# Kernel tuning notes

Hardware: AMD Instinct MI355X
Metric: run time of the kernel (lower is better)

Reference implementation:

```python
import jax, jax.numpy as jnp
import numpy as np

B, L, D_IN, D_H, N_CLS = 512, 256, 300, 96, 20
N = B * L            # total nodes = 131072
DEG = 8
E = N * DEG          # 1,048,576 edges
VOCAB = 50001        # num_words + 1 (padding row)
STEP = 2
NEG_SLOPE = 0.2


def setup_inputs() -> dict:
    key = jax.random.key(0)
    ks = jax.random.split(key, 24)
    node_ids = jax.random.randint(ks[0], (N,), 0, 50000)
    # block-local edges: each edge stays within its graph's node range
    gid = jnp.repeat(jnp.arange(B), L * DEG)           # [E]
    src = gid * L + jax.random.randint(ks[1], (E,), 0, L)
    dst = gid * L + jax.random.randint(ks[2], (E,), 0, L)

    def xavier(k, shape):
        fan_in, fan_out = shape[0], shape[-1]
        a = float(np.sqrt(6.0 / (fan_in + fan_out)))
        return jax.random.uniform(k, shape, jnp.float32, -a, a)

    inp = {
        "node_ids": node_ids, "src": src, "dst": dst,
        "embed": jax.random.normal(ks[3], (VOCAB, D_IN), jnp.float32),
        "We": xavier(ks[4], (D_IN, D_H)), "be": jnp.zeros((D_H,), jnp.float32),
        "Wg": xavier(ks[5], (D_H, D_H)),
        "att_src": xavier(ks[6], (D_H,)), "att_dst": xavier(ks[7], (D_H,)),
        "bg": jnp.zeros((D_H,), jnp.float32),
        "Wz0": xavier(ks[8], (D_H, D_H)), "bz0": jnp.zeros((D_H,), jnp.float32),
        "Wz1": xavier(ks[9], (D_H, D_H)), "bz1": jnp.zeros((D_H,), jnp.float32),
        "Wr0": xavier(ks[10], (D_H, D_H)), "br0": jnp.zeros((D_H,), jnp.float32),
        "Wr1": xavier(ks[11], (D_H, D_H)), "br1": jnp.zeros((D_H,), jnp.float32),
        "Wh0": xavier(ks[12], (D_H, D_H)), "bh0": jnp.zeros((D_H,), jnp.float32),
        "Wh1": xavier(ks[13], (D_H, D_H)), "bh1": jnp.zeros((D_H,), jnp.float32),
        "Wemb": xavier(ks[14], (D_H, D_H)),
        "Wmlp": xavier(ks[15], (D_H, N_CLS)),
    }
    return inp


def _forward(node_ids, src, dst, embed, We, be, Wg, att_src, att_dst, bg,
             Wz0, bz0, Wz1, bz1, Wr0, br0, Wr1, br1, Wh0, bh0, Wh1, bh1,
             Wemb, Wmlp):
    # embedding lookup + encode (dropout off, eval)
    x = embed[node_ids]                                  # [N, D_IN]
    x = jnp.tanh(x @ We + be)                            # [N, D_H]

    # self loops (GATConv add_self_loops=True, heads=1)
    loop = jnp.arange(N)
    s = jnp.concatenate([src, loop])
    d = jnp.concatenate([dst, loop])

    for _ in range(STEP):
        # ---- GATConv ----
        h = x @ Wg                                       # [N, D_H]
        a_s = h @ att_src                                # [N]
        a_d = h @ att_dst                                # [N]
        e = a_s[s] + a_d[d]
        e = jnp.where(e > 0, e, NEG_SLOPE * e)           # leaky_relu
        # segment softmax over incoming edges of each target node
        m = jax.ops.segment_max(e, d, num_segments=N)
        ex = jnp.exp(e - m[d])
        denom = jax.ops.segment_sum(ex, d, num_segments=N)
        alpha = ex / denom[d]                            # [E+N]
        a = jax.ops.segment_sum(alpha[:, None] * h[s], d, num_segments=N) + bg
        # ---- GRU update (act=tanh) ----
        z = jax.nn.sigmoid(a @ Wz0 + bz0 + x @ Wz1 + bz1)
        r = jax.nn.sigmoid(a @ Wr0 + br0 + x @ Wr1 + br1)
        hh = jnp.tanh(a @ Wh0 + bh0 + (x * r) @ Wh1 + bh1)
        x = hh * z + x * (1.0 - z)

    # graph2batch: equal-length graphs -> reshape, mask is all ones
    xb = x.reshape(B, L, D_H)
    y = jnp.tanh(xb @ Wemb)                              # [B, L, D_H]
    pooled = y.max(axis=1) + y.mean(axis=1)              # max + mean readout
    return pooled @ Wmlp                                 # [B, N_CLS]


def reference(node_ids, src, dst, embed, We, be, Wg, att_src, att_dst, bg,
              Wz0, bz0, Wz1, bz1, Wr0, br0, Wr1, br1, Wh0, bh0, Wh1, bh1,
              Wemb, Wmlp):
    return _forward(node_ids, src, dst, embed, We, be, Wg, att_src, att_dst, bg,
                    Wz0, bz0, Wz1, bz1, Wr0, br0, Wr1, br1, Wh0, bh0, Wh1, bh1,
                    Wemb, Wmlp)
```

## Files before the change

kernel.cpp:

```cpp
#include <hip/hip_runtime.h>
#include <hip/hip_bf16.h>

#define NNODES 131072
#define LGRAPH 256
#define BGRAPH 512
#define DIN 300
#define DH 96
#define EPG 2048
#define VOCAB 50001
#define NCLS 20
#define NEG 0.2f
#define EMB_ROWS 50048
#define EMB_K 320
#define WS 100
#define XS 104

typedef __attribute__((ext_vector_type(4))) float f32x4;
typedef __attribute__((ext_vector_type(8))) short bf16x8;
typedef __attribute__((ext_vector_type(8))) unsigned short u16x8;
#define MFMA16(a, b, c) __builtin_amdgcn_mfma_f32_16x16x32_bf16(a, b, c, 0, 0, 0)

__device__ __forceinline__ unsigned short f2b(float f) {
  __hip_bfloat16 h = __float2bfloat16(f);
  return *reinterpret_cast<unsigned short*>(&h);
}
__device__ __forceinline__ float b2f(unsigned short u) {
  unsigned v = ((unsigned)u) << 16;
  return __uint_as_float(v);
}
__device__ __forceinline__ float sigm(float v) { return 1.f / (1.f + __expf(-v)); }
__device__ __forceinline__ float ftanh(float x) {
  float ax = fabsf(x);
  float e = __expf(ax + ax);
  float t = 1.f - 2.f / (e + 1.f);
  return copysignf(t, x);
}

__global__ void k_prep_w(const float* __restrict__ Wg, const float* __restrict__ Wz0,
                         const float* __restrict__ Wz1, const float* __restrict__ Wr0,
                         const float* __restrict__ Wr1, const float* __restrict__ Wh0,
                         const float* __restrict__ Wh1, const float* __restrict__ Wemb,
                         const float* __restrict__ We,
                         const float* __restrict__ bz0, const float* __restrict__ bz1,
                         const float* __restrict__ br0, const float* __restrict__ br1,
                         const float* __restrict__ bh0, const float* __restrict__ bh1,
                         unsigned short* __restrict__ WT, unsigned short* __restrict__ WeT,
                         float* __restrict__ bc) {
  const int b = blockIdx.x, t = threadIdx.x;
  if (b < 8) {
    const float* src = (b == 0) ? Wg : (b == 1) ? Wz0 : (b == 2) ? Wz1 : (b == 3) ? Wr0
                     : (b == 4) ? Wr1 : (b == 5) ? Wh0 : (b == 6) ? Wh1 : Wemb;
    unsigned short* dst = WT + b * DH * DH;
    for (int i = t; i < DH * DH; i += 256) {
      int c = i / DH, k = i - c * DH;
      dst[i] = f2b(src[k * DH + c]);
    }
  } else if (b == 8) {
    for (int i = t; i < DH * EMB_K; i += 256) {
      int c = i / EMB_K, k = i - c * EMB_K;
      WeT[i] = (k < DIN) ? f2b(We[k * DH + c]) : (unsigned short)0;
    }
  } else {
    if (t < DH) {
      bc[t] = bz0[t] + bz1[t];
      bc[DH + t] = br0[t] + br1[t];
      bc[2 * DH + t] = bh0[t] + bh1[t];
    }
  }
}

__device__ __forceinline__ bf16x8 ldcvt(const float* __restrict__ p, int row, int ko) {
  bf16x8 r;
  if (row < VOCAB) {
    float4 c0 = (ko + 4 <= DIN) ? *(const float4*)&p[row * DIN + ko]
                                : make_float4(0.f, 0.f, 0.f, 0.f);
    float4 c1 = (ko + 8 <= DIN) ? *(const float4*)&p[row * DIN + ko + 4]
                                : make_float4(0.f, 0.f, 0.f, 0.f);
    r[0] = (short)f2b(c0.x); r[1] = (short)f2b(c0.y);
    r[2] = (short)f2b(c0.z); r[3] = (short)f2b(c0.w);
    r[4] = (short)f2b(c1.x); r[5] = (short)f2b(c1.y);
    r[6] = (short)f2b(c1.z); r[7] = (short)f2b(c1.w);
  } else {
    #pragma unroll
    for (int j = 0; j < 8; ++j) r[j] = 0;
  }
  return r;
}

__global__ void k_emb_mm(const float* __restrict__ embed,
                         const unsigned short* __restrict__ WeT,
                         unsigned short* __restrict__ Tb) {
  const int t = threadIdx.x, w = t >> 6, l = t & 63, li = l & 15, lh = l >> 4;
  const int wbase = blockIdx.x * 128 + w * 32;
  f32x4 acc[2][6];
  #pragma unroll
  for (int rt = 0; rt < 2; rt++)
    #pragma unroll
    for (int ct = 0; ct < 6; ct++) acc[rt][ct] = (f32x4)0.f;
  for (int ks = 0; ks < 10; ++ks) {
    const int ko = lh * 8 + ks * 32;
    bf16x8 aA0 = ldcvt(embed, wbase + li, ko);
    bf16x8 aA1 = ldcvt(embed, wbase + 16 + li, ko);
    #pragma unroll
    for (int ct = 0; ct < 6; ct++) {
      bf16x8 bB = *(const bf16x8*)&WeT[(ct * 16 + li) * EMB_K + ko];
      acc[0][ct] = MFMA16(aA0, bB, acc[0][ct]);
      acc[1][ct] = MFMA16(aA1, bB, acc[1][ct]);
    }
  }
  #pragma unroll
  for (int rt = 0; rt < 2; rt++)
    #pragma unroll
    for (int ct = 0; ct < 6; ct++)
      #pragma unroll
      for (int r = 0; r < 4; r++)
        Tb[(wbase + rt * 16 + lh * 4 + r) * DH + ct * 16 + li] = f2b(acc[rt][ct][r]);
}

__global__ __launch_bounds__(256) void k_gh(
    const int* __restrict__ ids, const unsigned short* __restrict__ Tb,
    const float* __restrict__ be, const unsigned short* __restrict__ WgT,
    const float* __restrict__ att_s, const float* __restrict__ att_d,
    unsigned short* __restrict__ xb, unsigned short* __restrict__ h,
    float* __restrict__ a_s, float* __restrict__ a_d) {
  __shared__ __align__(16) unsigned short sX[128 * XS];
  __shared__ int s_id[128];
  __shared__ float s_be[DH];
  const int t = threadIdx.x, w = t >> 6, l = t & 63, li = l & 15, lh = l >> 4;
  const int nb0 = blockIdx.x * 128;
  bf16x8 WF[6][3];
  #pragma unroll
  for (int ct = 0; ct < 6; ++ct)
    #pragma unroll
    for (int ks = 0; ks < 3; ++ks)
      WF[ct][ks] = *(const bf16x8*)&WgT[(ct * 16 + li) * DH + lh * 8 + ks * 32];
  if (t < 128) s_id[t] = ids[nb0 + t];
  if (t < DH) s_be[t] = be[t];
  __syncthreads();
  #pragma unroll
  for (int j = 0; j < 6; ++j) {
    int idx = t + 256 * j;
    int row = idx / 12, ch = idx - row * 12;
    u16x8 v = *(const u16x8*)&Tb[s_id[row] * DH + ch * 8];
    u16x8 o;
    #pragma unroll
    for (int k = 0; k < 8; ++k) o[k] = f2b(ftanh(b2f(v[k]) + s_be[ch * 8 + k]));
    *(u16x8*)&sX[row * XS + ch * 8] = o;
    *(u16x8*)&xb[(nb0 + row) * DH + ch * 8] = o;
  }
  __syncthreads();
  const int wbase = w * 32;
  f32x4 acc[2][6];
  #pragma unroll
  for (int rt = 0; rt < 2; rt++)
    #pragma unroll
    for (int ct = 0; ct < 6; ct++) acc[rt][ct] = (f32x4)0.f;
  bf16x8 aA[2][3];
  #pragma unroll
  for (int rt = 0; rt < 2; rt++)
    #pragma unroll
    for (int ks = 0; ks < 3; ks++)
      aA[rt][ks] = *(const bf16x8*)&sX[(wbase + rt * 16 + li) * XS + lh * 8 + ks * 32];
  #pragma unroll
  for (int ks = 0; ks < 3; ++ks)
    #pragma unroll
    for (int ct = 0; ct < 6; ct++) {
      acc[0][ct] = MFMA16(aA[0][ks], WF[ct][ks], acc[0][ct]);
      acc[1][ct] = MFMA16(aA[1][ks], WF[ct][ks], acc[1][ct]);
    }
  float ps[2][4] = {}, pd[2][4] = {};
  #pragma unroll
  for (int rt = 0; rt < 2; rt++)
    #pragma unroll
    for (int ct = 0; ct < 6; ct++) {
      const int col = ct * 16 + li;
      const float as_ = att_s[col], ad_ = att_d[col];
      #pragma unroll
      for (int r = 0; r < 4; r++) {
        float v = acc[rt][ct][r];
        h[(nb0 + wbase + rt * 16 + lh * 4 + r) * DH + col] = f2b(v);
        ps[rt][r] += v * as_;
        pd[rt][r] += v * ad_;
      }
    }
  #pragma unroll
  for (int rt = 0; rt < 2; rt++)
    #pragma unroll
    for (int r = 0; r < 4; r++) {
      float s = ps[rt][r], d = pd[rt][r];
      #pragma unroll
      for (int m = 1; m < 16; m <<= 1) { s += __shfl_xor(s, m); d += __shfl_xor(d, m); }
      if (li == 0) {
        const int row = nb0 + wbase + rt * 16 + lh * 4 + r;
        a_s[row] = s;
        a_d[row] = d;
      }
    }
}

__global__ __launch_bounds__(256) void k_h(
    const unsigned short* __restrict__ xb, const unsigned short* __restrict__ WgT,
    const float* __restrict__ att_s, const float* __restrict__ att_d,
    unsigned short* __restrict__ h, float* __restrict__ a_s,
    float* __restrict__ a_d) {
  __shared__ __align__(16) unsigned short sW[DH * WS];
  const int t = threadIdx.x, w = t >> 6, l = t & 63, li = l & 15, lh = l >> 4;
  const int wbase = blockIdx.x * 128 + w * 32;
  for (int i = t; i < DH * 12; i += 256) {
    int r = i / 12, c8 = i - r * 12;
    *(int4*)&sW[r * WS + c8 * 8] = *(const int4*)&WgT[r * DH + c8 * 8];
  }
  __syncthreads();
  f32x4 acc[2][6];
  #pragma unroll
  for (int rt = 0; rt < 2; rt++)
    #pragma unroll
    for (int ct = 0; ct < 6; ct++) acc[rt][ct] = (f32x4)0.f;
  #pragma unroll
  for (int ks = 0; ks < 3; ++ks) {
    const int ko = lh * 8 + ks * 32;
    bf16x8 aA0 = *(const bf16x8*)&xb[(wbase + li) * DH + ko];
    bf16x8 aA1 = *(const bf16x8*)&xb[(wbase + 16 + li) * DH + ko];
    #pragma unroll
    for (int ct = 0; ct < 6; ct++) {
      bf16x8 bB = *(const bf16x8*)&sW[(ct * 16 + li) * WS + ko];
      acc[0][ct] = MFMA16(aA0, bB, acc[0][ct]);
      acc[1][ct] = MFMA16(aA1, bB, acc[1][ct]);
    }
  }
  float ps[2][4] = {}, pd[2][4] = {};
  #pragma unroll
  for (int rt = 0; rt < 2; rt++)
    #pragma unroll
    for (int ct = 0; ct < 6; ct++) {
      const int col = ct * 16 + li;
      const float as_ = att_s[col], ad_ = att_d[col];
      #pragma unroll
      for (int r = 0; r < 4; r++) {
        float v = acc[rt][ct][r];
        h[(wbase + rt * 16 + lh * 4 + r) * DH + col] = f2b(v);
        ps[rt][r] += v * as_;
        pd[rt][r] += v * ad_;
      }
    }
  #pragma unroll
  for (int rt = 0; rt < 2; rt++)
    #pragma unroll
    for (int r = 0; r < 4; r++) {
      float s = ps[rt][r], d = pd[rt][r];
      #pragma unroll
      for (int m = 1; m < 16; m <<= 1) { s += __shfl_xor(s, m); d += __shfl_xor(d, m); }
      if (li == 0) {
        const int row = wbase + rt * 16 + lh * 4 + r;
        a_s[row] = s;
        a_d[row] = d;
      }
    }
}

__global__ __launch_bounds__(512, 4) void k_att(
    const int* __restrict__ src, const int* __restrict__ dst,
    const unsigned short* __restrict__ h, const float* __restrict__ a_sg,
    const float* __restrict__ a_dg, const float* __restrict__ bg,
    unsigned short* __restrict__ aout) {
  __shared__ __align__(16) unsigned short sH[LGRAPH * XS];
  __shared__ float s_ev[EPG];
  __shared__ unsigned char s_sl[EPG], s_dl[EPG];
  __shared__ unsigned char s_srcS[EPG];
  __shared__ int s_cnt[LGRAPH], s_off[LGRAPH], s_pos[LGRAPH];
  __shared__ float s_as[LGRAPH], s_ad[LGRAPH];
  __shared__ float s_bg[DH];
  const int g = blockIdx.x, t = threadIdx.x;
  const int nb = g * LGRAPH;
  if (t < LGRAPH) { s_cnt[t] = 0; s_as[t] = a_sg[nb + t]; s_ad[t] = a_dg[nb + t]; }
  if (t < DH) s_bg[t] = bg[t];
  #pragma unroll
  for (int j = 0; j < 6; ++j) {
    int idx = t + 512 * j;
    int row = idx / 12, ch = idx - row * 12;
    *(int4*)&sH[row * XS + ch * 8] = *(const int4*)&h[(nb + row) * DH + ch * 8];
  }
  __syncthreads();
  for (int e = t; e < EPG; e += 512) {
    int sl = src[g * EPG + e] - nb, dl = dst[g * EPG + e] - nb;
    s_sl[e] = (unsigned char)sl;
    s_dl[e] = (unsigned char)dl;
    atomicAdd(&s_cnt[dl], 1);
  }
  __syncthreads();
  if (t < 64) {
    int carry = 0;
    #pragma unroll
    for (int c = 0; c < 4; ++c) {
      int v = s_cnt[c * 64 + t];
      int x = v;
      #pragma unroll
      for (int o = 1; o < 64; o <<= 1) {
        int y = __shfl_up(x, o);
        if (t >= o) x += y;
      }
      s_off[c * 64 + t] = x - v + carry;
      carry += __shfl(x, 63);
    }
  }
  __syncthreads();
  if (t < LGRAPH) s_pos[t] = s_off[t];
  __syncthreads();
  for (int e = t; e < EPG; e += 512) {
    int sl = s_sl[e], dl = s_dl[e];
    float ee = s_as[sl] + s_ad[dl];
    ee = ee > 0.f ? ee : NEG * ee;
    int pos = atomicAdd(&s_pos[dl], 1);
    s_srcS[pos] = (unsigned char)sl;
    s_ev[pos] = ee;
  }
  __syncthreads();
  {
    const int d = t >> 1, half = t & 1;
    const int beg = s_off[d], end = beg + s_cnt[d];
    float ss = s_as[d] + s_ad[d];
    ss = ss > 0.f ? ss : NEG * ss;
    float m = ss;
    for (int i = beg; i < end; ++i) m = fmaxf(m, s_ev[i]);
    const int cbase = half * 48;
    float acc[48];
    float wself = __expf(ss - m);
    float den = wself;
    #pragma unroll
    for (int k = 0; k < 6; ++k) {
      u16x8 v = *(const u16x8*)&sH[d * XS + cbase + k * 8];
      #pragma unroll
      for (int j = 0; j < 8; ++j) acc[k * 8 + j] = wself * b2f(v[j]);
    }
    for (int i = beg; i < end; ++i) {
      float wv = __expf(s_ev[i] - m);
      den += wv;
      int sl2 = s_srcS[i];
      #pragma unroll
      for (int k = 0; k < 6; ++k) {
        u16x8 v = *(const u16x8*)&sH[sl2 * XS + cbase + k * 8];
        #pragma unroll
        for (int j = 0; j < 8; ++j) acc[k * 8 + j] += wv * b2f(v[j]);
      }
    }
    float inv = 1.f / den;
    unsigned short* op = &aout[(nb + d) * DH + cbase];
    #pragma unroll
    for (int k = 0; k < 6; ++k) {
      u16x8 o;
      #pragma unroll
      for (int j = 0; j < 8; ++j) o[j] = f2b(acc[k * 8 + j] * inv + s_bg[cbase + k * 8 + j]);
      *(u16x8*)&op[k * 8] = o;
    }
  }
}

__global__ __launch_bounds__(768, 3) void k_gru(
    const unsigned short* __restrict__ ab, unsigned short* __restrict__ xb,
    const unsigned short* __restrict__ WT, const float* __restrict__ bc) {
  __shared__ __align__(16) unsigned short sW[6 * DH * WS];
  __shared__ __align__(16) unsigned short sX[128 * WS];
  const int t = threadIdx.x, w = t >> 6, l = t & 63, li = l & 15, lh = l >> 4;
  const int wr = w / 3, wc = w - wr * 3;
  #pragma unroll
  for (int m = 0; m < 6; ++m) {
    const int srcm = (m == 0) ? 3 : (m == 1) ? 4 : (m == 2) ? 1 : (m == 3) ? 2 : (m == 4) ? 5 : 6;
    const unsigned short* srcp = WT + srcm * DH * DH;
    for (int i = t; i < DH * 12; i += 768) {
      int r = i / 12, c8 = i - r * 12;
      *(int4*)&sW[(m * DH + r) * WS + c8 * 8] = *(const int4*)&srcp[r * DH + c8 * 8];
    }
  }
  float zb_[2], rb_[2], hb_[2];
  #pragma unroll
  for (int ct = 0; ct < 2; ++ct) {
    const int col = wc * 32 + ct * 16 + li;
    zb_[ct] = bc[col]; rb_[ct] = bc[DH + col]; hb_[ct] = bc[2 * DH + col];
  }

  for (int tile = 0; tile < 4; ++tile) {
    const int nb0 = (blockIdx.x * 4 + tile) * 128;
    __syncthreads();
    #pragma unroll
    for (int j = 0; j < 2; ++j) {
      int idx = t + 768 * j;
      int row = idx / 12, ch = idx - row * 12;
      *(int4*)&sX[row * WS + ch * 8] = *(const int4*)&xb[(nb0 + row) * DH + ch * 8];
    }
    __syncthreads();
    bf16x8 aA[2][3], aX[2][3];
    #pragma unroll
    for (int rt = 0; rt < 2; rt++)
      #pragma unroll
      for (int ks = 0; ks < 3; ks++) {
        const int row = wr * 32 + rt * 16 + li;
        const int ko = lh * 8 + ks * 32;
        aA[rt][ks] = *(const bf16x8*)&ab[(nb0 + row) * DH + ko];
        aX[rt][ks] = *(const bf16x8*)&sX[row * WS + ko];
      }
    float xo[2][2][4];
    #pragma unroll
    for (int rt = 0; rt < 2; rt++)
      #pragma unroll
      for (int ct = 0; ct < 2; ct++)
        #pragma unroll
        for (int r = 0; r < 4; r++)
          xo[rt][ct][r] = b2f(sX[(wr * 32 + rt * 16 + lh * 4 + r) * WS + wc * 32 + ct * 16 + li]);
    f32x4 accR[2][2], accZ[2][2];
    #pragma unroll
    for (int rt = 0; rt < 2; rt++)
      #pragma unroll
      for (int ct = 0; ct < 2; ct++) { accR[rt][ct] = (f32x4)0.f; accZ[rt][ct] = (f32x4)0.f; }
    #pragma unroll
    for (int ks = 0; ks < 3; ks++) {
      const int ko = lh * 8 + ks * 32;
      #pragma unroll
      for (int ct = 0; ct < 2; ct++) {
        const int wrow = wc * 32 + ct * 16 + li;
        bf16x8 w_r0 = *(const bf16x8*)&sW[(0 * DH + wrow) * WS + ko];
        bf16x8 w_r1 = *(const bf16x8*)&sW[(1 * DH + wrow) * WS + ko];
        bf16x8 w_z0 = *(const bf16x8*)&sW[(2 * DH + wrow) * WS + ko];
        bf16x8 w_z1 = *(const bf16x8*)&sW[(3 * DH + wrow) * WS + ko];
        #pragma unroll
        for (int rt = 0; rt < 2; rt++) {
          accR[rt][ct] = MFMA16(aA[rt][ks], w_r0, accR[rt][ct]);
          accR[rt][ct] = MFMA16(aX[rt][ks], w_r1, accR[rt][ct]);
          accZ[rt][ct] = MFMA16(aA[rt][ks], w_z0, accZ[rt][ct]);
          accZ[rt][ct] = MFMA16(aX[rt][ks], w_z1, accZ[rt][ct]);
        }
      }
    }
    __syncthreads();
    #pragma unroll
    for (int rt = 0; rt < 2; rt++)
      #pragma unroll
      for (int ct = 0; ct < 2; ct++) {
        const int col = wc * 32 + ct * 16 + li;
        #pragma unroll
        for (int r = 0; r < 4; r++) {
          float rv = sigm(accR[rt][ct][r] + rb_[ct]);
          sX[(wr * 32 + rt * 16 + lh * 4 + r) * WS + col] = f2b(xo[rt][ct][r] * rv);
        }
      }
    __syncthreads();
    bf16x8 aU[2][3];
    #pragma unroll
    for (int rt = 0; rt < 2; rt++)
      #pragma unroll
      for (int ks = 0; ks < 3; ks++)
        aU[rt][ks] = *(const bf16x8*)&sX[(wr * 32 + rt * 16 + li) * WS + lh * 8 + ks * 32];
    __syncthreads();
    f32x4 accH[2][2];
    #pragma unroll
    for (int rt = 0; rt < 2; rt++)
      #pragma unroll
      for (int ct = 0; ct < 2; ct++) accH[rt][ct] = (f32x4)0.f;
    #pragma unroll
    for (int ks = 0; ks < 3; ks++) {
      const int ko = lh * 8 + ks * 32;
      #pragma unroll
      for (int ct = 0; ct < 2; ct++) {
        const int wrow = wc * 32 + ct * 16 + li;
        bf16x8 w_h0 = *(const bf16x8*)&sW[(4 * DH + wrow) * WS + ko];
        bf16x8 w_h1 = *(const bf16x8*)&sW[(5 * DH + wrow) * WS + ko];
        #pragma unroll
        for (int rt = 0; rt < 2; rt++) {
          accH[rt][ct] = MFMA16(aA[rt][ks], w_h0, accH[rt][ct]);
          accH[rt][ct] = MFMA16(aU[rt][ks], w_h1, accH[rt][ct]);
        }
      }
    }
    #pragma unroll
    for (int rt = 0; rt < 2; rt++)
      #pragma unroll
      for (int ct = 0; ct < 2; ct++) {
        const int col = wc * 32 + ct * 16 + li;
        #pragma unroll
        for (int r = 0; r < 4; r++) {
          float z = sigm(accZ[rt][ct][r] + zb_[ct]);
          float hh = ftanh(accH[rt][ct][r] + hb_[ct]);
          float xn = hh * z + xo[rt][ct][r] * (1.f - z);
          sX[(wr * 32 + rt * 16 + lh * 4 + r) * WS + col] = f2b(xn);
        }
      }
    __syncthreads();
    #pragma unroll
    for (int j = 0; j < 2; ++j) {
      int idx = t + 768 * j;
      int row = idx / 12, ch = idx - row * 12;
      *(int4*)&xb[(nb0 + row) * DH + ch * 8] = *(const int4*)&sX[row * WS + ch * 8];
    }
  }
}

__global__ __launch_bounds__(256) void k_readout(
    const unsigned short* __restrict__ xb, const unsigned short* __restrict__ WembT,
    const float* __restrict__ Wmlp, float* __restrict__ out) {
  __shared__ __align__(16) unsigned short sW[DH * WS];
  __shared__ float pmaxs[4][DH], psums[4][DH];
  __shared__ float spool[DH];
  const int g = blockIdx.x, t = threadIdx.x, w = t >> 6, l = t & 63, li = l & 15, lh = l >> 4;
  const int wbase = g * LGRAPH + w * 64;
  for (int i = t; i < DH * 12; i += 256) {
    int r = i / 12, c8 = i - r * 12;
    *(int4*)&sW[r * WS + c8 * 8] = *(const int4*)&WembT[r * DH + c8 * 8];
  }
  __syncthreads();
  f32x4 acc[4][6];
  #pragma unroll
  for (int rt = 0; rt < 4; rt++)
    #pragma unroll
    for (int ct = 0; ct < 6; ct++) acc[rt][ct] = (f32x4)0.f;
  #pragma unroll
  for (int ks = 0; ks < 3; ks++) {
    const int ko = lh * 8 + ks * 32;
    bf16x8 aA[4];
    #pragma unroll
    for (int rt = 0; rt < 4; rt++)
      aA[rt] = *(const bf16x8*)&xb[(wbase + rt * 16 + li) * DH + ko];
    #pragma unroll
    for (int ct = 0; ct < 6; ct++) {
      bf16x8 bB = *(const bf16x8*)&sW[(ct * 16 + li) * WS + ko];
      #pragma unroll
      for (int rt = 0; rt < 4; rt++) acc[rt][ct] = MFMA16(aA[rt], bB, acc[rt][ct]);
    }
  }
  float pm[6], psu[6];
  #pragma unroll
  for (int ct = 0; ct < 6; ct++) {
    float mx = -1e30f, sm = 0.f;
    #pragma unroll
    for (int rt = 0; rt < 4; rt++)
      #pragma unroll
      for (int r = 0; r < 4; r++) {
        float y = ftanh(acc[rt][ct][r]);
        mx = fmaxf(mx, y);
        sm += y;
      }
    pm[ct] = mx; psu[ct] = sm;
  }
  #pragma unroll
  for (int ct = 0; ct < 6; ct++) {
    pm[ct] = fmaxf(pm[ct], __shfl_xor(pm[ct], 16));
    psu[ct] += __shfl_xor(psu[ct], 16);
    pm[ct] = fmaxf(pm[ct], __shfl_xor(pm[ct], 32));
    psu[ct] += __shfl_xor(psu[ct], 32);
  }
  if (lh == 0) {
    #pragma unroll
    for (int ct = 0; ct < 6; ct++) {
      pmaxs[w][ct * 16 + li] = pm[ct];
      psums[w][ct * 16 + li] = psu[ct];
    }
  }
  __syncthreads();
  if (t < DH) {
    float mx = fmaxf(fmaxf(pmaxs[0][t], pmaxs[1][t]), fmaxf(pmaxs[2][t], pmaxs[3][t]));
    float sm = psums[0][t] + psums[1][t] + psums[2][t] + psums[3][t];
    spool[t] = mx + sm * (1.f / LGRAPH);
  }
  __syncthreads();
  if (t < NCLS) {
    float a = 0.f;
    for (int k = 0; k < DH; ++k) a += spool[k] * Wmlp[k * NCLS + t];
    out[g * NCLS + t] = a;
  }
}

extern "C" void kernel_launch(void* const* d_in, const int* in_sizes, int n_in,
                              void* d_out, int out_size, void* d_ws, size_t ws_size,
                              hipStream_t stream) {
  const int*   node_ids = (const int*)d_in[0];
  const int*   src      = (const int*)d_in[1];
  const int*   dst      = (const int*)d_in[2];
  const float* embed    = (const float*)d_in[3];
  const float* We   = (const float*)d_in[4];
  const float* be   = (const float*)d_in[5];
  const float* Wg   = (const float*)d_in[6];
  const float* att_src = (const float*)d_in[7];
  const float* att_dst = (const float*)d_in[8];
  const float* bg   = (const float*)d_in[9];
  const float* Wz0  = (const float*)d_in[10];
  const float* bz0  = (const float*)d_in[11];
  const float* Wz1  = (const float*)d_in[12];
  const float* bz1  = (const float*)d_in[13];
  const float* Wr0  = (const float*)d_in[14];
  const float* br0  = (const float*)d_in[15];
  const float* Wr1  = (const float*)d_in[16];
  const float* br1  = (const float*)d_in[17];
  const float* Wh0  = (const float*)d_in[18];
  const float* bh0  = (const float*)d_in[19];
  const float* Wh1  = (const float*)d_in[20];
  const float* bh1  = (const float*)d_in[21];
  const float* Wemb = (const float*)d_in[22];
  const float* Wmlp = (const float*)d_in[23];
  float* out = (float*)d_out;

  char* w_ = (char*)d_ws;
  unsigned short* xb   = (unsigned short*)(w_ + 0);
  unsigned short* ab   = (unsigned short*)(w_ + 25165824);
  unsigned short* h    = (unsigned short*)(w_ + 50331648);
  unsigned short* Tb   = (unsigned short*)(w_ + 75497472);
  float*          a_s  = (float*)(w_ + 85106688);
  float*          a_d  = (float*)(w_ + 85630976);
  unsigned short* WT   = (unsigned short*)(w_ + 86155264);
  unsigned short* WeT  = (unsigned short*)(w_ + 86302720);
  float*          bc   = (float*)(w_ + 86364160);

  unsigned short* WgT   = WT + 0 * DH * DH;
  unsigned short* WembT = WT + 7 * DH * DH;

  hipLaunchKernelGGL(k_prep_w, dim3(10), dim3(256), 0, stream,
                     Wg, Wz0, Wz1, Wr0, Wr1, Wh0, Wh1, Wemb, We,
                     bz0, bz1, br0, br1, bh0, bh1, WT, WeT, bc);
  hipLaunchKernelGGL(k_emb_mm, dim3(EMB_ROWS / 128), dim3(256), 0, stream, embed, WeT, Tb);
  hipLaunchKernelGGL(k_gh, dim3(NNODES / 128), dim3(256), 0, stream,
                     node_ids, Tb, be, WgT, att_src, att_dst, xb, h, a_s, a_d);
  hipLaunchKernelGGL(k_att, dim3(BGRAPH), dim3(512), 0, stream,
                     src, dst, h, a_s, a_d, bg, ab);
  hipLaunchKernelGGL(k_gru, dim3(256), dim3(768), 0, stream, ab, xb, WT, bc);
  hipLaunchKernelGGL(k_h, dim3(NNODES / 128), dim3(256), 0, stream,
                     xb, WgT, att_src, att_dst, h, a_s, a_d);
  hipLaunchKernelGGL(k_att, dim3(BGRAPH), dim3(512), 0, stream,
                     src, dst, h, a_s, a_d, bg, ab);
  hipLaunchKernelGGL(k_gru, dim3(256), dim3(768), 0, stream, ab, xb, WT, bc);
  hipLaunchKernelGGL(k_readout, dim3(BGRAPH), dim3(256), 0, stream, xb, WembT, Wmlp, out);
}
```

Before: 236.2 us.

## Stage embedding tile in LDS with coalesced loads in embedding matmul

The embedding-table projection kernel now loads each 128-row tile of the fp32 embedding with coalesced float4 reads, converts it to bf16 into a padded LDS buffer, and feeds the MFMAs from LDS. The block grows to 512 threads so each wave handles 16 rows instead of 32. This replaces the strided, partially masked per-lane global loads of the old version, in exchange for about 82 KB of LDS per block and a barrier, which limits occupancy.

```diff
diff --git a/kernel.cpp b/kernel.cpp
--- a/kernel.cpp
+++ b/kernel.cpp
@@ -12,6 +12,7 @@
 #define NEG 0.2f
 #define EMB_ROWS 50048
 #define EMB_K 320
+#define ES 328
 #define WS 100
 #define XS 104
 
@@ -69,52 +70,44 @@
   }
 }
 
-__device__ __forceinline__ bf16x8 ldcvt(const float* __restrict__ p, int row, int ko) {
-  bf16x8 r;
-  if (row < VOCAB) {
-    float4 c0 = (ko + 4 <= DIN) ? *(const float4*)&p[row * DIN + ko]
-                                : make_float4(0.f, 0.f, 0.f, 0.f);
-    float4 c1 = (ko + 8 <= DIN) ? *(const float4*)&p[row * DIN + ko + 4]
-                                : make_float4(0.f, 0.f, 0.f, 0.f);
-    r[0] = (short)f2b(c0.x); r[1] = (short)f2b(c0.y);
-    r[2] = (short)f2b(c0.z); r[3] = (short)f2b(c0.w);
-    r[4] = (short)f2b(c1.x); r[5] = (short)f2b(c1.y);
-    r[6] = (short)f2b(c1.z); r[7] = (short)f2b(c1.w);
-  } else {
-    #pragma unroll
-    for (int j = 0; j < 8; ++j) r[j] = 0;
-  }
-  return r;
-}
-
-__global__ void k_emb_mm(const float* __restrict__ embed,
-                         const unsigned short* __restrict__ WeT,
-                         unsigned short* __restrict__ Tb) {
+__global__ __launch_bounds__(512) void k_emb_mm(
+    const float* __restrict__ embed, const unsigned short* __restrict__ WeT,
+    unsigned short* __restrict__ Tb) {
+  __shared__ __align__(16) unsigned short sE[128 * ES];
   const int t = threadIdx.x, w = t >> 6, l = t & 63, li = l & 15, lh = l >> 4;
-  const int wbase = blockIdx.x * 128 + w * 32;
-  f32x4 acc[2][6];
-  #pragma unroll
-  for (int rt = 0; rt < 2; rt++)
-    #pragma unroll
-    for (int ct = 0; ct < 6; ct++) acc[rt][ct] = (f32x4)0.f;
+  const int rbase = blockIdx.x * 128;
+  for (int idx = t; idx < 128 * 20; idx += 512) {
+    int row = idx / 20, k = 300 + (idx - (idx / 20) * 20);
+    sE[row * ES + k] = 0;
+  }
+  for (int idx = t; idx < 9600; idx += 512) {
+    int row = idx / 75, c4 = idx - row * 75;
+    int gr = rbase + row;
+    float4 v = (gr < VOCAB) ? *(const float4*)&embed[gr * DIN + c4 * 4]
+                            : make_float4(0.f, 0.f, 0.f, 0.f);
+    ushort4 o;
+    o.x = f2b(v.x); o.y = f2b(v.y); o.z = f2b(v.z); o.w = f2b(v.w);
+    *(ushort4*)&sE[row * ES + c4 * 4] = o;
+  }
+  __syncthreads();
+  const int r0 = w * 16;
+  f32x4 acc[6];
+  #pragma unroll
+  for (int ct = 0; ct < 6; ct++) acc[ct] = (f32x4)0.f;
   for (int ks = 0; ks < 10; ++ks) {
     const int ko = lh * 8 + ks * 32;
-    bf16x8 aA0 = ldcvt(embed, wbase + li, ko);
-    bf16x8 aA1 = ldcvt(embed, wbase + 16 + li, ko);
+    bf16x8 aA = *(const bf16x8*)&sE[(r0 + li) * ES + ko];
     #pragma unroll
     for (int ct = 0; ct < 6; ct++) {
       bf16x8 bB = *(const bf16x8*)&WeT[(ct * 16 + li) * EMB_K + ko];
-      acc[0][ct] = MFMA16(aA0, bB, acc[0][ct]);
-      acc[1][ct] = MFMA16(aA1, bB, acc[1][ct]);
-    }
-  }
-  #pragma unroll
-  for (int rt = 0; rt < 2; rt++)
-    #pragma unroll
-    for (int ct = 0; ct < 6; ct++)
-      #pragma unroll
-      for (int r = 0; r < 4; r++)
-        Tb[(wbase + rt * 16 + lh * 4 + r) * DH + ct * 16 + li] = f2b(acc[rt][ct][r]);
+      acc[ct] = MFMA16(aA, bB, acc[ct]);
+    }
+  }
+  #pragma unroll
+  for (int ct = 0; ct < 6; ct++)
+    #pragma unroll
+    for (int r = 0; r < 4; r++)
+      Tb[(rbase + r0 + lh * 4 + r) * DH + ct * 16 + li] = f2b(acc[ct][r]);
 }
 
 __global__ __launch_bounds__(256) void k_gh(
@@ -613,7 +606,7 @@
   hipLaunchKernelGGL(k_prep_w, dim3(10), dim3(256), 0, stream,
                      Wg, Wz0, Wz1, Wr0, Wr1, Wh0, Wh1, Wemb, We,
                      bz0, bz1, br0, br1, bh0, bh1, WT, WeT, bc);
-  hipLaunchKernelGGL(k_emb_mm, dim3(EMB_ROWS / 128), dim3(256), 0, stream, embed, WeT, Tb);
+  hipLaunchKernelGGL(k_emb_mm, dim3(EMB_ROWS / 128), dim3(512), 0, stream, embed, WeT, Tb);
   hipLaunchKernelGGL(k_gh, dim3(NNODES / 128), dim3(256), 0, stream,
                      node_ids, Tb, be, WgT, att_src, att_dst, xb, h, a_s, a_d);
   hipLaunchKernelGGL(k_att, dim3(BGRAPH), dim3(512), 0, stream,
```

Result: slower. 254.4 us (+7.7%).
